# Performance work log

Hardware: AMD Instinct MI355X
Metric: run time of the kernel (lower is better)

Reference implementation:

```python
import jax, jax.numpy as jnp
import numpy as np

BLK = 128          # block size for fp8 block-wise scales
FP8_MAX = 448.0    # max representable magnitude of float8_e4m3fn


def _dequant_act(a, s):
    # a: (E, M, K) fp8 values stored in fp32; s: (E, M, K//BLK) per-token 1x128 scales
    E, M, K = a.shape
    nb = K // BLK
    return (a.reshape(E, M, nb, BLK) * s[..., None]).reshape(E, M, K)


def _dequant_w(w, s):
    # w: (E, N, K) fp8 values stored in fp32; s: (E, N//BLK, K//BLK) 128x128 block scales
    E, N, K = w.shape
    return (w.reshape(E, N // BLK, BLK, K // BLK, BLK) * s[:, :, None, :, None]).reshape(E, N, K)


def _fp8_round(x):
    # round-to-fp8(e4m3fn) with straight-through value semantics
    q = x.astype(jnp.float8_e4m3fn).astype(jnp.float32)
    return x + jax.lax.stop_gradient(q - x)


def setup_inputs() -> dict:
    key = jax.random.key(0)
    ks = jax.random.split(key, 8)
    E, N, K, M = 8, 2048, 4096, 1024
    f8 = lambda x: x.astype(jnp.float8_e4m3fn).astype(jnp.float32)
    hidden_states_fp8 = f8(jax.random.normal(ks[0], (E, M, K), dtype=jnp.float32))
    hidden_states_scale = jax.random.uniform(ks[1], (E, M, K // BLK), dtype=jnp.float32, minval=0.01, maxval=1.0)
    masked_m = jax.random.randint(ks[2], (E,), 1, M + 1, dtype=jnp.int32)
    w13_weight_fp8 = f8(jax.random.normal(ks[3], (E, N, K), dtype=jnp.float32))
    w13_weight_scale = jax.random.uniform(ks[4], (E, N // BLK, K // BLK), dtype=jnp.float32, minval=0.01, maxval=1.0)
    w2_weight_fp8 = f8(jax.random.normal(ks[5], (E, K, N // 2), dtype=jnp.float32))
    w2_weight_scale = jax.random.uniform(ks[6], (E, K // BLK, N // 2 // BLK), dtype=jnp.float32, minval=0.01, maxval=1.0)
    return {
        "hidden_states_fp8": hidden_states_fp8,
        "hidden_states_scale": hidden_states_scale,
        "masked_m": masked_m,
        "expected_m": 512,
        "w13_weight_fp8": w13_weight_fp8,
        "w13_weight_scale": w13_weight_scale,
        "w2_weight_fp8": w2_weight_fp8,
        "w2_weight_scale": w2_weight_scale,
    }


def reference(hidden_states_fp8, hidden_states_scale, masked_m, expected_m,
              w13_weight_fp8, w13_weight_scale, w2_weight_fp8, w2_weight_scale):
    E, M, K = hidden_states_fp8.shape
    # per-expert row validity mask (rows >= masked_m[e] are padding)
    mask = jnp.arange(M)[None, :] < masked_m[:, None]            # (E, M)

    # --- grouped GEMM 1: (x @ w13^T) -> bf16, masked by valid rows ---
    a = _dequant_act(hidden_states_fp8, hidden_states_scale)     # (E, M, K)
    w13 = _dequant_w(w13_weight_fp8, w13_weight_scale)           # (E, N, K)
    gateup = jnp.einsum('emk,enk->emn', a, w13)
    gateup = gateup.astype(jnp.bfloat16).astype(jnp.float32)     # gemm emits bf16

    # --- fused SiLU * mul + per-128-block fp8 quantization ---
    gate, up = jnp.split(gateup, 2, axis=-1)                     # (E, M, N/2) each
    x = jax.nn.silu(gate) * up
    x = jnp.where(mask[..., None], x, 0.0)
    N2 = x.shape[-1]
    nb = N2 // BLK
    xb = x.reshape(E, M, nb, BLK)
    amax = jnp.max(jnp.abs(xb), axis=-1)                         # (E, M, nb)
    scale = jnp.maximum(amax, 1e-10) / FP8_MAX
    q = _fp8_round(xb / scale[..., None])                        # fp8-rounded values
    a2 = (q * scale[..., None]).reshape(E, M, N2)                # dequantized for gemm 2

    # --- grouped GEMM 2: (down_input @ w2^T) -> bf16 ---
    w2 = _dequant_w(w2_weight_fp8, w2_weight_scale)              # (E, K, N/2)
    out = jnp.einsum('emn,ekn->emk', a2, w2).astype(jnp.bfloat16)
    out = jnp.where(mask[..., None], out, jnp.bfloat16(0))
    return out
```

## Files before the change

kernel.cpp:

```cpp
#include <hip/hip_runtime.h>
#include <hip/hip_bf16.h>

#define E_  8
#define M_  1024
#define K_  4096
#define N_  2048
#define N2_ 1024

typedef unsigned short u16;
typedef unsigned int   u32;

typedef __bf16 bf16x8 __attribute__((ext_vector_type(8)));
typedef float  f32x4  __attribute__((ext_vector_type(4)));

union FragU { uint4 u; bf16x8 v; };

__device__ __forceinline__ u16 f2bfu(float f){
  union { __hip_bfloat16 h; u16 u; } c;
  c.h = __float2bfloat16(f);
  return c.u;
}
__device__ __forceinline__ u32 pack2(float a, float b){
  return (u32)f2bfu(a) | ((u32)f2bfu(b) << 16);
}
__device__ __forceinline__ float bf2f(u16 u){
  u32 x = ((u32)u) << 16;
  return __uint_as_float(x);
}
__device__ __forceinline__ float bf16val(float f){
  return bf2f(f2bfu(f));
}
__device__ __forceinline__ float fp8_round(float x){
  float ax = fabsf(x);
  if (ax < 0.015625f){
    return rintf(x * 512.0f) * (1.0f/512.0f);
  }
  u32 u = __float_as_uint(x);
  u32 lsb = (u >> 20) & 1u;
  u += 0x7FFFFu + lsb;
  u &= 0xFFF00000u;
  return __uint_as_float(u);
}

template<int AMODE, int KD, int ND>
__global__ __launch_bounds__(256, 2) void gemm_grouped(
    const void* __restrict__ Aptr_, const float* __restrict__ Ascale,
    const float* __restrict__ Bptr, const float* __restrict__ Wscale,
    const int* __restrict__ masked_m, void* __restrict__ Cout)
{
  constexpr int BK  = 64;
  constexpr int KT  = KD / BK;
  constexpr int NKB = KD / 128;
  const int tn = blockIdx.x, tm = blockIdx.y, e = blockIdx.z;
  const int m0 = tm * 128, n0 = tn * 128;
  const int me = masked_m[e];
  const int tid = threadIdx.x;

  u16*   const Cu = (u16*)Cout;
  float* const Cf = (float*)Cout;

  if (m0 >= me){
    if constexpr (AMODE == 1){
      const uint4 z = make_uint4(0u,0u,0u,0u);
      #pragma unroll
      for (int q = 0; q < 16; ++q){
        int idx = tid + 256*q;
        int r = idx >> 5, c = idx & 31;
        *reinterpret_cast<uint4*>(Cf + ((size_t)e*M_ + m0 + r)*ND + n0 + c*4) = z;
      }
    }
    return;
  }

  __shared__ u16 sA[2][128*64];
  __shared__ u16 sB[2][128*64];

  const int rrow = tid >> 3;
  const int kq   = tid & 7;
  const float* Af = (const float*)Aptr_;
  const u16*   Au = (const u16*)Aptr_;

  float4 rA[8], rB[8];
  uint4  rAu[4];
  float  rAs[4];
  float  sWv = 0.f;

  auto STAGE_LOAD = [&](int kt){
    const int k0 = kt * BK;
    const int kb = k0 >> 7;
    sWv = Wscale[((size_t)e*(ND/128) + tn)*NKB + kb];
    #pragma unroll
    for (int p = 0; p < 4; ++p){
      const int r = p*32 + rrow;
      if constexpr (AMODE == 0){
        const float* ap = Af + ((size_t)e*M_ + m0 + r)*KD + k0 + kq*8;
        rA[2*p]   = *reinterpret_cast<const float4*>(ap);
        rA[2*p+1] = *reinterpret_cast<const float4*>(ap + 4);
        rAs[p]    = Ascale[((size_t)e*M_ + m0 + r)*NKB + kb];
      } else {
        const u16* ap = Au + ((size_t)e*M_ + m0 + r)*KD + k0 + kq*8;
        rAu[p] = *reinterpret_cast<const uint4*>(ap);
      }
      const float* bp = Bptr + ((size_t)e*ND + n0 + r)*KD + k0 + kq*8;
      rB[2*p]   = *reinterpret_cast<const float4*>(bp);
      rB[2*p+1] = *reinterpret_cast<const float4*>(bp + 4);
    }
  };

  auto STAGE_WRITE = [&](int buf){
    #pragma unroll
    for (int p = 0; p < 4; ++p){
      const int r   = p*32 + rrow;
      const int dst = r*64 + ((kq ^ (r & 7)) * 8);
      if constexpr (AMODE == 0){
        const float s = rAs[p];
        uint4 w;
        w.x = pack2(rA[2*p].x * s,   rA[2*p].y * s);
        w.y = pack2(rA[2*p].z * s,   rA[2*p].w * s);
        w.z = pack2(rA[2*p+1].x * s, rA[2*p+1].y * s);
        w.w = pack2(rA[2*p+1].z * s, rA[2*p+1].w * s);
        *reinterpret_cast<uint4*>(&sA[buf][dst]) = w;
      } else {
        *reinterpret_cast<uint4*>(&sA[buf][dst]) = rAu[p];
      }
      uint4 wb;
      wb.x = pack2(rB[2*p].x * sWv,   rB[2*p].y * sWv);
      wb.y = pack2(rB[2*p].z * sWv,   rB[2*p].w * sWv);
      wb.z = pack2(rB[2*p+1].x * sWv, rB[2*p+1].y * sWv);
      wb.w = pack2(rB[2*p+1].z * sWv, rB[2*p+1].w * sWv);
      *reinterpret_cast<uint4*>(&sB[buf][dst]) = wb;
    }
  };

  const int lane = tid & 63, wid = tid >> 6;
  const int wm = wid >> 1, wn = wid & 1;
  const int fr = lane & 15, kg = lane >> 4;

  f32x4 acc[4][4];
  #pragma unroll
  for (int i = 0; i < 4; ++i)
    #pragma unroll
    for (int j = 0; j < 4; ++j)
      acc[i][j] = (f32x4){0.f, 0.f, 0.f, 0.f};

  auto COMPUTE = [&](int buf){
    #pragma unroll
    for (int ks = 0; ks < 2; ++ks){
      FragU av[4], bv[4];
      #pragma unroll
      for (int i = 0; i < 4; ++i){
        const int r  = wm*64 + i*16 + fr;
        const int ch = (ks*4 + kg) ^ (r & 7);
        av[i].u = *reinterpret_cast<const uint4*>(&sA[buf][r*64 + ch*8]);
      }
      #pragma unroll
      for (int j = 0; j < 4; ++j){
        const int r  = wn*64 + j*16 + fr;
        const int ch = (ks*4 + kg) ^ (r & 7);
        bv[j].u = *reinterpret_cast<const uint4*>(&sB[buf][r*64 + ch*8]);
      }
      #pragma unroll
      for (int i = 0; i < 4; ++i)
        #pragma unroll
        for (int j = 0; j < 4; ++j)
          acc[i][j] = __builtin_amdgcn_mfma_f32_16x16x32_bf16(av[i].v, bv[j].v, acc[i][j], 0, 0, 0);
    }
  };

  STAGE_LOAD(0);
  STAGE_WRITE(0);
  __syncthreads();
  int cur = 0;
  for (int kt = 0; kt < KT; ++kt){
    if (kt + 1 < KT) STAGE_LOAD(kt + 1);
    COMPUTE(cur);
    if (kt + 1 < KT) STAGE_WRITE(cur ^ 1);
    __syncthreads();
    cur ^= 1;
  }

  #pragma unroll
  for (int i = 0; i < 4; ++i){
    #pragma unroll
    for (int j = 0; j < 4; ++j){
      #pragma unroll
      for (int r = 0; r < 4; ++r){
        const int gm = m0 + wm*64 + i*16 + kg*4 + r;
        const int gn = n0 + wn*64 + j*16 + fr;
        if constexpr (AMODE == 0){
          if (gm < me) Cu[((size_t)e*M_ + gm)*ND + gn] = f2bfu(acc[i][j][r]);
        } else {
          const float v = (gm < me) ? bf16val(acc[i][j][r]) : 0.0f;
          Cf[((size_t)e*M_ + gm)*ND + gn] = v;
        }
      }
    }
  }
}

__global__ __launch_bounds__(128) void act_quant_kernel(
    const u16* __restrict__ gu, const int* __restrict__ masked_m,
    u16* __restrict__ a2)
{
  const int m = blockIdx.x, e = blockIdx.y;
  if (m >= masked_m[e]) return;
  const int t = threadIdx.x;
  const u16* row = gu + ((size_t)e*M_ + m)*N_;
  uint4 g4 = *reinterpret_cast<const uint4*>(row + t*8);
  uint4 u4 = *reinterpret_cast<const uint4*>(row + N2_ + t*8);
  u32 gp[4] = {g4.x, g4.y, g4.z, g4.w};
  u32 up[4] = {u4.x, u4.y, u4.z, u4.w};

  float x[8];
  #pragma unroll
  for (int w = 0; w < 4; ++w){
    float g0 = bf2f((u16)(gp[w] & 0xffffu));
    float g1 = bf2f((u16)(gp[w] >> 16));
    float u0 = bf2f((u16)(up[w] & 0xffffu));
    float u1 = bf2f((u16)(up[w] >> 16));
    x[2*w]   = g0 / (1.0f + expf(-g0)) * u0;
    x[2*w+1] = g1 / (1.0f + expf(-g1)) * u1;
  }

  float amax = 0.f;
  #pragma unroll
  for (int k = 0; k < 8; ++k) amax = fmaxf(amax, fabsf(x[k]));
  #pragma unroll
  for (int o = 8; o > 0; o >>= 1) amax = fmaxf(amax, __shfl_xor(amax, o, 16));
  const float scale = fmaxf(amax, 1e-10f) / 448.0f;

  u32 hh[4];
  #pragma unroll
  for (int w = 0; w < 4; ++w){
    float d0 = fp8_round(x[2*w]   / scale) * scale;
    float d1 = fp8_round(x[2*w+1] / scale) * scale;
    hh[w] = pack2(d0, d1);
  }
  uint4 o4 = make_uint4(hh[0], hh[1], hh[2], hh[3]);
  *reinterpret_cast<uint4*>(a2 + ((size_t)e*M_ + m)*N2_ + t*8) = o4;
}

extern "C" void kernel_launch(void* const* d_in, const int* in_sizes, int n_in,
                              void* d_out, int out_size, void* d_ws, size_t ws_size,
                              hipStream_t stream)
{
  const float* hs   = (const float*)d_in[0];
  const float* hss  = (const float*)d_in[1];
  const int*   mm   = (const int*)d_in[2];
  const float* w13  = (const float*)d_in[4];
  const float* w13s = (const float*)d_in[5];
  const float* w2   = (const float*)d_in[6];
  const float* w2s  = (const float*)d_in[7];

  u16* gu = (u16*)d_out;
  u16* a2 = (u16*)d_ws;

  gemm_grouped<0, K_, N_><<<dim3(N_/128, M_/128, E_), dim3(256), 0, stream>>>(
      hs, hss, w13, w13s, mm, gu);
  act_quant_kernel<<<dim3(M_, E_), dim3(128), 0, stream>>>(gu, mm, a2);
  gemm_grouped<1, N2_, K_><<<dim3(K_/128, M_/128, E_), dim3(256), 0, stream>>>(
      a2, nullptr, w2, w2s, mm, d_out);
}
```

Baseline: 365.6 us.

## Pre-convert activations to swizzled bf16 and load A tiles via direct global-to-LDS

Adds a pre-pass that dequantizes the fp32 hidden states into a pre-swizzled bf16 buffer. The activation-quant kernel now also writes its output in the same swizzled order. Both GEMMs then stream the A tile straight into LDS with global_load_lds, which removes the register staging and in-loop scaling for A. This halves the A bytes read inside the GEMM, where each A tile is re-read by every N tile. The cost is an extra kernel and an extra write and read of the bf16 activation buffer, which lives in spare space of the output buffer.

Result: faster. 331.6 us (-9.3%).

```diff
diff --git a/kernel.cpp b/kernel.cpp
--- a/kernel.cpp
+++ b/kernel.cpp
@@ -42,11 +42,35 @@
   return __uint_as_float(u);
 }
 
+#define GLD16(g, l) __builtin_amdgcn_global_load_lds( \
+    (const __attribute__((address_space(1))) void*)(g), \
+    (__attribute__((address_space(3))) void*)(l), 16, 0, 0)
+
+__global__ __launch_bounds__(512) void conv_hs_kernel(
+    const float* __restrict__ hs, const float* __restrict__ hss,
+    const int* __restrict__ masked_m, u16* __restrict__ hs16)
+{
+  const int m = blockIdx.x, e = blockIdx.y;
+  if (m >= masked_m[e]) return;
+  const int c = threadIdx.x;
+  const float s = hss[((size_t)e*M_ + m)*(K_/128) + (c >> 4)];
+  const float* src = hs + ((size_t)e*M_ + m)*K_ + c*8;
+  const float4 f0 = *reinterpret_cast<const float4*>(src);
+  const float4 f1 = *reinterpret_cast<const float4*>(src + 4);
+  uint4 w;
+  w.x = pack2(f0.x * s, f0.y * s);
+  w.y = pack2(f0.z * s, f0.w * s);
+  w.z = pack2(f1.x * s, f1.y * s);
+  w.w = pack2(f1.z * s, f1.w * s);
+  const int cd = (c & ~7) | ((c & 7) ^ (m & 7));
+  *reinterpret_cast<uint4*>(hs16 + ((size_t)e*M_ + m)*K_ + cd*8) = w;
+}
+
 template<int AMODE, int KD, int ND>
 __global__ __launch_bounds__(256, 2) void gemm_grouped(
-    const void* __restrict__ Aptr_, const float* __restrict__ Ascale,
-    const float* __restrict__ Bptr, const float* __restrict__ Wscale,
-    const int* __restrict__ masked_m, void* __restrict__ Cout)
+    const u16* __restrict__ Abf, const float* __restrict__ Bptr,
+    const float* __restrict__ Wscale, const int* __restrict__ masked_m,
+    void* __restrict__ Cout)
 {
   constexpr int BK  = 64;
   constexpr int KT  = KD / BK;
@@ -75,54 +99,42 @@
   __shared__ u16 sA[2][128*64];
   __shared__ u16 sB[2][128*64];
 
+  const int lane = tid & 63, wid = tid >> 6;
   const int rrow = tid >> 3;
   const int kq   = tid & 7;
-  const float* Af = (const float*)Aptr_;
-  const u16*   Au = (const u16*)Aptr_;
-
-  float4 rA[8], rB[8];
-  uint4  rAu[4];
-  float  rAs[4];
+
+  float4 rB[8];
   float  sWv = 0.f;
 
-  auto STAGE_LOAD = [&](int kt){
+  auto ISSUE_A = [&](int kt, int buf){
+    const int k0 = kt * BK;
+    #pragma unroll
+    for (int q = 0; q < 4; ++q){
+      const int ins = wid*4 + q;
+      const int r   = ins*8 + (lane >> 3);
+      const u16* src = Abf + ((size_t)e*M_ + m0 + r)*KD + k0 + (lane & 7)*8;
+      GLD16(src, &sA[buf][ins*512]);
+    }
+  };
+
+  auto LOAD_B = [&](int kt){
     const int k0 = kt * BK;
     const int kb = k0 >> 7;
     sWv = Wscale[((size_t)e*(ND/128) + tn)*NKB + kb];
     #pragma unroll
     for (int p = 0; p < 4; ++p){
       const int r = p*32 + rrow;
-      if constexpr (AMODE == 0){
-        const float* ap = Af + ((size_t)e*M_ + m0 + r)*KD + k0 + kq*8;
-        rA[2*p]   = *reinterpret_cast<const float4*>(ap);
-        rA[2*p+1] = *reinterpret_cast<const float4*>(ap + 4);
-        rAs[p]    = Ascale[((size_t)e*M_ + m0 + r)*NKB + kb];
-      } else {
-        const u16* ap = Au + ((size_t)e*M_ + m0 + r)*KD + k0 + kq*8;
-        rAu[p] = *reinterpret_cast<const uint4*>(ap);
-      }
       const float* bp = Bptr + ((size_t)e*ND + n0 + r)*KD + k0 + kq*8;
       rB[2*p]   = *reinterpret_cast<const float4*>(bp);
       rB[2*p+1] = *reinterpret_cast<const float4*>(bp + 4);
     }
   };
 
-  auto STAGE_WRITE = [&](int buf){
+  auto WRITE_B = [&](int buf){
     #pragma unroll
     for (int p = 0; p < 4; ++p){
       const int r   = p*32 + rrow;
       const int dst = r*64 + ((kq ^ (r & 7)) * 8);
-      if constexpr (AMODE == 0){
-        const float s = rAs[p];
-        uint4 w;
-        w.x = pack2(rA[2*p].x * s,   rA[2*p].y * s);
-        w.y = pack2(rA[2*p].z * s,   rA[2*p].w * s);
-        w.z = pack2(rA[2*p+1].x * s, rA[2*p+1].y * s);
-        w.w = pack2(rA[2*p+1].z * s, rA[2*p+1].w * s);
-        *reinterpret_cast<uint4*>(&sA[buf][dst]) = w;
-      } else {
-        *reinterpret_cast<uint4*>(&sA[buf][dst]) = rAu[p];
-      }
       uint4 wb;
       wb.x = pack2(rB[2*p].x * sWv,   rB[2*p].y * sWv);
       wb.y = pack2(rB[2*p].z * sWv,   rB[2*p].w * sWv);
@@ -132,7 +144,6 @@
     }
   };
 
-  const int lane = tid & 63, wid = tid >> 6;
   const int wm = wid >> 1, wn = wid & 1;
   const int fr = lane & 15, kg = lane >> 4;
 
@@ -167,14 +178,18 @@
     }
   };
 
-  STAGE_LOAD(0);
-  STAGE_WRITE(0);
+  ISSUE_A(0, 0);
+  LOAD_B(0);
+  WRITE_B(0);
   __syncthreads();
   int cur = 0;
   for (int kt = 0; kt < KT; ++kt){
-    if (kt + 1 < KT) STAGE_LOAD(kt + 1);
+    if (kt + 1 < KT){
+      ISSUE_A(kt + 1, cur ^ 1);
+      LOAD_B(kt + 1);
+    }
     COMPUTE(cur);
-    if (kt + 1 < KT) STAGE_WRITE(cur ^ 1);
+    if (kt + 1 < KT) WRITE_B(cur ^ 1);
     __syncthreads();
     cur ^= 1;
   }
@@ -237,7 +252,8 @@
     hh[w] = pack2(d0, d1);
   }
   uint4 o4 = make_uint4(hh[0], hh[1], hh[2], hh[3]);
-  *reinterpret_cast<uint4*>(a2 + ((size_t)e*M_ + m)*N2_ + t*8) = o4;
+  const int td = (t & ~7) | ((t & 7) ^ (m & 7));
+  *reinterpret_cast<uint4*>(a2 + ((size_t)e*M_ + m)*N2_ + td*8) = o4;
 }
 
 extern "C" void kernel_launch(void* const* d_in, const int* in_sizes, int n_in,
@@ -252,12 +268,14 @@
   const float* w2   = (const float*)d_in[6];
   const float* w2s  = (const float*)d_in[7];
 
-  u16* gu = (u16*)d_out;
-  u16* a2 = (u16*)d_ws;
-
+  u16* gu   = (u16*)d_out;
+  u16* hs16 = (u16*)d_out + (size_t)E_*M_*N_;
+  u16* a2   = (u16*)d_ws;
+
+  conv_hs_kernel<<<dim3(M_, E_), dim3(512), 0, stream>>>(hs, hss, mm, hs16);
   gemm_grouped<0, K_, N_><<<dim3(N_/128, M_/128, E_), dim3(256), 0, stream>>>(
-      hs, hss, w13, w13s, mm, gu);
+      hs16, w13, w13s, mm, gu);
   act_quant_kernel<<<dim3(M_, E_), dim3(128), 0, stream>>>(gu, mm, a2);
   gemm_grouped<1, N2_, K_><<<dim3(K_/128, M_/128, E_), dim3(256), 0, stream>>>(
-      a2, nullptr, w2, w2s, mm, d_out);
-}
+      a2, w2, w2s, mm, d_out);
+}
```
